# Performance work log

Hardware: AMD Instinct MI355X
Metric: run time of the kernel (lower is better)

Reference implementation:

```python
import jax, jax.numpy as jnp
import numpy as np

N_NODES = 50000
N_EDGES = 625000
H_FEATS = 128


def setup_inputs() -> dict:
    key = jax.random.key(0)
    k_h, k_src, k_dst, k_w1, k_w2 = jax.random.split(key, 5)
    h = jax.random.normal(k_h, (N_NODES, H_FEATS), dtype=jnp.float32)
    src = jax.random.randint(k_src, (N_EDGES,), 0, N_NODES, dtype=jnp.int64)
    dst = jax.random.randint(k_dst, (N_EDGES,), 0, N_NODES, dtype=jnp.int64)
    # Linear weights stored as (in, out) for x @ W + b
    lim1 = 1.0 / np.sqrt(2 * H_FEATS)
    lim2 = 1.0 / np.sqrt(H_FEATS)
    W1 = jax.random.uniform(k_w1, (2 * H_FEATS, H_FEATS), jnp.float32, -lim1, lim1)
    b1 = jnp.zeros((H_FEATS,), jnp.float32)
    W2 = jax.random.uniform(k_w2, (H_FEATS, 1), jnp.float32, -lim2, lim2)
    b2 = jnp.zeros((1,), jnp.float32)
    return {"h": h, "src": src, "dst": dst, "W1": W1, "b1": b1, "W2": W2, "b2": b2}


def reference(h, src, dst, W1, b1, W2, b2):
    # Gather source/destination node features per edge, concat, 2-layer MLP.
    he = jnp.concatenate([h[src], h[dst]], axis=1)          # [E, 2*H]
    hid = jax.nn.relu(he @ W1 + b1)                          # [E, H]
    score = (hid @ W2 + b2)[:, 0]                            # [E]
    return score
```

## Files before the change

### kernel.cpp

```cpp
#include <hip/hip_runtime.h>
#include <hip/hip_bf16.h>

#define N_NODES   50000
#define N_EDGES   625000
#define HF        128
#define MTILE     64
#define NTILES    ((N_EDGES + MTILE - 1) / MTILE)
#define NROWTILES (N_NODES / 16)
#define HB_BYTES  ((size_t)N_NODES * HF * sizeof(short))
#define W1F_BYTES ((size_t)4096 * 16)
#define UVQ_BYTES ((size_t)N_NODES * 256)
#define SCL_BYTES ((size_t)N_NODES * 8)
#define WS_NEED   (W1F_BYTES + UVQ_BYTES + SCL_BYTES)

typedef __attribute__((ext_vector_type(8))) short s16x8;
typedef __attribute__((ext_vector_type(4))) float f32x4;
typedef __attribute__((ext_vector_type(4))) unsigned int u32x4;

__device__ __forceinline__ short f2bf(float x) {
    unsigned u = __builtin_bit_cast(unsigned, x);
    u += 0x7FFFu + ((u >> 16) & 1u);
    return (short)(u >> 16);
}
__device__ __forceinline__ float bf2f(short s) {
    return __builtin_bit_cast(float, ((unsigned)(unsigned short)s) << 16);
}

__global__ void conv_w_kernel(const float* __restrict__ W1, short* __restrict__ w1f) {
    int j = blockIdx.x * 256 + threadIdx.x;
    if (j < 4096) {
        const int lr  = j & 15;
        const int lg  = (j >> 4) & 3;
        const int ntg = (j >> 6) & 15;
        const int kt  = j >> 10;
        const int n2  = ntg * 16 + lr;
        const int kb  = kt * 32 + lg * 8;
        const float* wp = (n2 < 128) ? (W1 + (size_t)kb * 128 + n2)
                                     : (W1 + (size_t)(kb + 128) * 128 + (n2 - 128));
        s16x8 f;
        #pragma unroll
        for (int i = 0; i < 8; ++i) f[i] = f2bf(wp[(size_t)i * 128]);
        ((s16x8*)w1f)[j] = f;
    }
}

__global__ __launch_bounds__(256, 3) void uv_gemm7_kernel(
    const float* __restrict__ h,
    const short* __restrict__ w1f,
    const float* __restrict__ b1,
    unsigned char* __restrict__ UVq,
    float2* __restrict__ scl)
{
    __shared__ short ldsA[16 * 128];
    __shared__ float rm[4][16];
    __shared__ __align__(16) char qt[16][272];

    const int t  = threadIdx.x;
    const int w  = t >> 6;
    const int l  = t & 63;
    const int lg = l >> 4;
    const int lr = l & 15;
    const int srow = t >> 4;
    const int sch  = t & 15;
    const int side = w >> 1;

    s16x8 bfrag[4][4];
    #pragma unroll
    for (int kt = 0; kt < 4; ++kt)
        #pragma unroll
        for (int nt = 0; nt < 4; ++nt)
            bfrag[kt][nt] = ((const s16x8*)w1f)[(kt * 16 + w * 4 + nt) * 64 + l];

    float b1v[4];
    #pragma unroll
    for (int nt = 0; nt < 4; ++nt)
        b1v[nt] = 0.5f * b1[(w * 64 + nt * 16 + lr) & 127];

    int tile = blockIdx.x;
    f32x4 pa, pb;
    {
        int gr = tile * 16 + srow; if (gr > N_NODES - 1) gr = N_NODES - 1;
        const float* hp = h + (size_t)gr * HF + sch * 8;
        pa = *reinterpret_cast<const f32x4*>(hp);
        pb = *reinterpret_cast<const f32x4*>(hp + 4);
    }

    while (tile < NROWTILES) {
        const int R0 = tile * 16;
        {
            s16x8 p;
            p[0]=f2bf(pa[0]); p[1]=f2bf(pa[1]); p[2]=f2bf(pa[2]); p[3]=f2bf(pa[3]);
            p[4]=f2bf(pb[0]); p[5]=f2bf(pb[1]); p[6]=f2bf(pb[2]); p[7]=f2bf(pb[3]);
            *reinterpret_cast<s16x8*>((char*)ldsA + srow * 256 + ((sch * 16) ^ ((srow & 7) << 4))) = p;
        }
        const int next = tile + gridDim.x;
        if (next < NROWTILES) {
            int gr = next * 16 + srow; if (gr > N_NODES - 1) gr = N_NODES - 1;
            const float* hp = h + (size_t)gr * HF + sch * 8;
            pa = *reinterpret_cast<const f32x4*>(hp);
            pb = *reinterpret_cast<const f32x4*>(hp + 4);
        }
        __syncthreads();

        s16x8 afr[4];
        #pragma unroll
        for (int kt = 0; kt < 4; ++kt)
            afr[kt] = *reinterpret_cast<const s16x8*>(
                (char*)ldsA + lr * 256 + ((kt * 64 + lg * 16) ^ ((lr & 7) << 4)));

        f32x4 acc[4];
        #pragma unroll
        for (int nt = 0; nt < 4; ++nt) acc[nt] = (f32x4){0.f, 0.f, 0.f, 0.f};
        #pragma unroll
        for (int kt = 0; kt < 4; ++kt)
            #pragma unroll
            for (int nt = 0; nt < 4; ++nt)
                acc[nt] = __builtin_amdgcn_mfma_f32_16x16x32_bf16(afr[kt], bfrag[kt][nt], acc[nt], 0, 0, 0);

        float val[4][4];
        float am[4];
        #pragma unroll
        for (int rr = 0; rr < 4; ++rr) am[rr] = 0.f;
        #pragma unroll
        for (int nt = 0; nt < 4; ++nt)
            #pragma unroll
            for (int rr = 0; rr < 4; ++rr) {
                float v = acc[nt][rr] + b1v[nt];
                val[nt][rr] = v;
                float a = fabsf(v);
                am[rr] = a > am[rr] ? a : am[rr];
            }
        #pragma unroll
        for (int m = 1; m <= 8; m <<= 1)
            #pragma unroll
            for (int rr = 0; rr < 4; ++rr) {
                float o = __shfl_xor(am[rr], m, 64);
                am[rr] = o > am[rr] ? o : am[rr];
            }
        if (lr == 0) {
            #pragma unroll
            for (int rr = 0; rr < 4; ++rr) rm[w][lg * 4 + rr] = am[rr];
        }
        __syncthreads();

        #pragma unroll
        for (int rr = 0; rr < 4; ++rr) {
            const int row = lg * 4 + rr;
            const float rmax = fmaxf(rm[side * 2][row], rm[side * 2 + 1][row]);
            const float inv = rmax > 0.f ? 127.f / rmax : 0.f;
            #pragma unroll
            for (int nt = 0; nt < 4; ++nt) {
                int q = (int)rintf(val[nt][rr] * inv) + 128;
                q = q < 0 ? 0 : (q > 255 ? 255 : q);
                qt[row][w * 64 + nt * 16 + lr] = (char)q;
            }
        }
        if (t < 16) {
            const float sU = fmaxf(rm[0][t], rm[1][t]) * (1.f / 127.f);
            const float sV = fmaxf(rm[2][t], rm[3][t]) * (1.f / 127.f);
            const int grow = R0 + t;
            if (grow < N_NODES) {
                float2 s2; s2.x = sU; s2.y = sV;
                scl[grow] = s2;
            }
        }
        __syncthreads();

        {
            const int row = t >> 4, ch = t & 15;
            const int grow = R0 + row;
            if (grow < N_NODES) {
                u32x4 vv = *reinterpret_cast<const u32x4*>(&qt[row][ch * 16]);
                *reinterpret_cast<u32x4*>(UVq + (size_t)grow * 256 + ch * 16) = vv;
            }
        }
        __syncthreads();
        tile = next;
    }
}

__device__ __forceinline__ float dot16q(u32x4 u, u32x4 v, float su, float sv,
                                        const float* w2) {
    const float off = -128.f * (su + sv);
    float a = 0.f;
    #pragma unroll
    for (int q = 0; q < 4; ++q) {
        const unsigned uu = u[q], vv = v[q];
        #pragma unroll
        for (int b = 0; b < 4; ++b) {
            const float cu = (float)((uu >> (8 * b)) & 255u);
            const float cv = (float)((vv >> (8 * b)) & 255u);
            float tt = fmaf(su, cu, fmaf(sv, cv, off));
            tt = tt > 0.f ? tt : 0.f;
            a = fmaf(tt, w2[q * 4 + b], a);
        }
    }
    return a;
}

__global__ __launch_bounds__(256) void edge_combine6_kernel(
    const unsigned char* __restrict__ UVq,
    const float2* __restrict__ scl,
    const int*   __restrict__ src,
    const int*   __restrict__ dst,
    const float* __restrict__ W2,
    const float* __restrict__ b2,
    float* __restrict__ out)
{
    const int t  = threadIdx.x;
    const int w  = t >> 6;
    const int l  = t & 63;
    const int eg = l >> 3;
    const int dg = l & 7;

    float w2v[16];
    #pragma unroll
    for (int j = 0; j < 16; ++j) w2v[j] = W2[dg * 16 + j];
    const float b2v = b2[0];

    const int gw = blockIdx.x * 4 + w;
    const int stride = gridDim.x * 4 * 32;

    int base = gw * 32;
    int jj0 = base + (l & 31); if (jj0 > N_EDGES - 1) jj0 = N_EDGES - 1;
    int ids = (l < 32) ? src[jj0] : dst[jj0];

    for (; base < N_EDGES; base += stride) {
        const float2 sc2 = scl[ids];
        const float sval = (l < 32) ? sc2.x : sc2.y;

        const int s0 = __shfl(ids, 0 * 8 + eg, 64), d0 = __shfl(ids, 32 + 0 * 8 + eg, 64);
        const int s1 = __shfl(ids, 1 * 8 + eg, 64), d1 = __shfl(ids, 32 + 1 * 8 + eg, 64);
        const int s2 = __shfl(ids, 2 * 8 + eg, 64), d2 = __shfl(ids, 32 + 2 * 8 + eg, 64);
        const int s3 = __shfl(ids, 3 * 8 + eg, 64), d3 = __shfl(ids, 32 + 3 * 8 + eg, 64);

        u32x4 uq0 = *(const u32x4*)(UVq + (size_t)s0 * 256 + dg * 16);
        u32x4 vq0 = *(const u32x4*)(UVq + (size_t)d0 * 256 + 128 + dg * 16);
        u32x4 uq1 = *(const u32x4*)(UVq + (size_t)s1 * 256 + dg * 16);
        u32x4 vq1 = *(const u32x4*)(UVq + (size_t)d1 * 256 + 128 + dg * 16);
        u32x4 uq2 = *(const u32x4*)(UVq + (size_t)s2 * 256 + dg * 16);
        u32x4 vq2 = *(const u32x4*)(UVq + (size_t)d2 * 256 + 128 + dg * 16);
        u32x4 uq3 = *(const u32x4*)(UVq + (size_t)s3 * 256 + dg * 16);
        u32x4 vq3 = *(const u32x4*)(UVq + (size_t)d3 * 256 + 128 + dg * 16);

        const int nb = base + stride;
        if (nb < N_EDGES) {
            int j2 = nb + (l & 31); if (j2 > N_EDGES - 1) j2 = N_EDGES - 1;
            ids = (l < 32) ? src[j2] : dst[j2];
        }
        __builtin_amdgcn_sched_barrier(0);

        const float su0 = __shfl(sval, 0 * 8 + eg, 64), sv0 = __shfl(sval, 32 + 0 * 8 + eg, 64);
        const float su1 = __shfl(sval, 1 * 8 + eg, 64), sv1 = __shfl(sval, 32 + 1 * 8 + eg, 64);
        const float su2 = __shfl(sval, 2 * 8 + eg, 64), sv2 = __shfl(sval, 32 + 2 * 8 + eg, 64);
        const float su3 = __shfl(sval, 3 * 8 + eg, 64), sv3 = __shfl(sval, 32 + 3 * 8 + eg, 64);

        float a0 = dot16q(uq0, vq0, su0, sv0, w2v);
        float a1 = dot16q(uq1, vq1, su1, sv1, w2v);
        float a2 = dot16q(uq2, vq2, su2, sv2, w2v);
        float a3 = dot16q(uq3, vq3, su3, sv3, w2v);

        #pragma unroll
        for (int m = 1; m <= 4; m <<= 1) {
            a0 += __shfl_xor(a0, m, 64);
            a1 += __shfl_xor(a1, m, 64);
            a2 += __shfl_xor(a2, m, 64);
            a3 += __shfl_xor(a3, m, 64);
        }

        if (dg == 0) {
            if (base + 0 * 8 + eg < N_EDGES) __builtin_nontemporal_store(a0 + b2v, &out[base + 0 * 8 + eg]);
            if (base + 1 * 8 + eg < N_EDGES) __builtin_nontemporal_store(a1 + b2v, &out[base + 1 * 8 + eg]);
            if (base + 2 * 8 + eg < N_EDGES) __builtin_nontemporal_store(a2 + b2v, &out[base + 2 * 8 + eg]);
            if (base + 3 * 8 + eg < N_EDGES) __builtin_nontemporal_store(a3 + b2v, &out[base + 3 * 8 + eg]);
        }
    }
}

__global__ void conv_h_kernel(const float* __restrict__ h, short* __restrict__ hb) {
    int i = blockIdx.x * blockDim.x + threadIdx.x;
    const int n8 = N_NODES * HF / 8;
    if (i < n8) {
        f32x4 a = ((const f32x4*)h)[i * 2];
        f32x4 b = ((const f32x4*)h)[i * 2 + 1];
        s16x8 p;
        p[0]=f2bf(a[0]); p[1]=f2bf(a[1]); p[2]=f2bf(a[2]); p[3]=f2bf(a[3]);
        p[4]=f2bf(b[0]); p[5]=f2bf(b[1]); p[6]=f2bf(b[2]); p[7]=f2bf(b[3]);
        ((s16x8*)hb)[i] = p;
    }
}

__device__ __forceinline__ void gatherA(const short* __restrict__ hb,
                                        int sid, int did, int lg, s16x8 (&A)[8]) {
    const s16x8* bs = (const s16x8*)(hb + (size_t)sid * HF);
    const s16x8* bd = (const s16x8*)(hb + (size_t)did * HF);
    A[0] = bs[lg];      A[1] = bs[4 + lg];  A[2] = bs[8 + lg];  A[3] = bs[12 + lg];
    A[4] = bd[lg];      A[5] = bd[4 + lg];  A[6] = bd[8 + lg];  A[7] = bd[12 + lg];
}

__device__ __forceinline__ void step_tile_v2(
    int tile, int g,
    const short* __restrict__ hb,
    const int* __restrict__ src, const int* __restrict__ dst,
    s16x8 (&Acur)[8], s16x8 (&Anext)[8],
    int sidg, int didg, int& sid2, int& did2,
    const s16x8 (&bfrag)[8][4],
    const float (&b1v)[4], const float (&w2v)[4], float b2v,
    float* __restrict__ out,
    float (&lds_p)[2][2][MTILE], int pp,
    int t, int r, int c, int lg, int lr, int myrow)
{
    gatherA(hb, sidg, didg, lg, Anext);
    {
        int e = (tile + 2 * g) * MTILE + myrow;
        e = e < N_EDGES ? e : N_EDGES - 1;
        sid2 = src[e]; did2 = dst[e];
    }
    f32x4 acc[4];
    #pragma unroll
    for (int nt = 0; nt < 4; ++nt) acc[nt] = (f32x4){0.f, 0.f, 0.f, 0.f};
    #pragma unroll
    for (int kt = 0; kt < 8; ++kt)
        #pragma unroll
        for (int nt = 0; nt < 4; ++nt)
            acc[nt] = __builtin_amdgcn_mfma_f32_16x16x32_bf16(Acur[kt], bfrag[kt][nt], acc[nt], 0, 0, 0);

    float s0[4];
    #pragma unroll
    for (int rr = 0; rr < 4; ++rr) {
        float a = 0.f;
        #pragma unroll
        for (int nt = 0; nt < 4; ++nt) {
            float v = acc[nt][rr] + b1v[nt];
            v = v > 0.f ? v : 0.f;
            a += v * w2v[nt];
        }
        s0[rr] = a;
    }
    #pragma unroll
    for (int mask = 1; mask <= 8; mask <<= 1)
        #pragma unroll
        for (int rr = 0; rr < 4; ++rr)
            s0[rr] += __shfl_xor(s0[rr], mask, 64);

    if (lr == 0) {
        #pragma unroll
        for (int rr = 0; rr < 4; ++rr)
            lds_p[pp][c][r * 16 + lg * 4 + rr] = s0[rr];
    }
    asm volatile("s_waitcnt lgkmcnt(0)" ::: "memory");
    __builtin_amdgcn_s_barrier();
    asm volatile("" ::: "memory");

    if (t < MTILE) {
        int e = tile * MTILE + t;
        if (e < N_EDGES)
            out[e] = lds_p[pp][0][t] + lds_p[pp][1][t] + b2v;
    }
}

__global__ __launch_bounds__(512, 2) void mlp_edge_score_v2(
    const short* __restrict__ hb,
    const int*   __restrict__ src,
    const int*   __restrict__ dst,
    const float* __restrict__ W1,
    const float* __restrict__ b1,
    const float* __restrict__ W2,
    const float* __restrict__ b2,
    float* __restrict__ out)
{
    __shared__ float lds_p[2][2][MTILE];

    const int t  = threadIdx.x;
    const int w  = t >> 6;
    const int l  = t & 63;
    const int r  = w >> 1;
    const int c  = w & 1;
    const int lg = l >> 4;
    const int lr = l & 15;
    const int myrow = r * 16 + lr;

    s16x8 bfrag[8][4];
    #pragma unroll
    for (int kt = 0; kt < 8; ++kt)
        #pragma unroll
        for (int nt = 0; nt < 4; ++nt) {
            const int n  = c * 64 + nt * 16 + lr;
            const int kb = kt * 32 + lg * 8;
            s16x8 f;
            #pragma unroll
            for (int i = 0; i < 8; ++i) f[i] = f2bf(W1[(size_t)(kb + i) * HF + n]);
            bfrag[kt][nt] = f;
        }
    float b1v[4], w2v[4];
    #pragma unroll
    for (int nt = 0; nt < 4; ++nt) {
        const int n = c * 64 + nt * 16 + lr;
        b1v[nt] = b1[n];
        w2v[nt] = W2[n];
    }
    const float b2v = b2[0];

    const int g = gridDim.x;
    const int tile0 = blockIdx.x;

    s16x8 Aa[8], Ab[8];
    {
        int e = tile0 * MTILE + myrow;
        e = e < N_EDGES ? e : N_EDGES - 1;
        gatherA(hb, src[e], dst[e], lg, Aa);
    }
    int sidA, didA, sidB, didB;
    {
        int e = (tile0 + g) * MTILE + myrow;
        e = e < N_EDGES ? e : N_EDGES - 1;
        sidA = src[e]; didA = dst[e];
    }

    int pp = 0;
    for (int tile = tile0; tile < NTILES; tile += 2 * g) {
        step_tile_v2(tile, g, hb, src, dst, Aa, Ab, sidA, didA, sidB, didB,
                     bfrag, b1v, w2v, b2v, out, lds_p, pp, t, r, c, lg, lr, myrow);
        pp ^= 1;
        if (tile + g < NTILES) {
            step_tile_v2(tile + g, g, hb, src, dst, Ab, Aa, sidB, didB, sidA, didA,
                         bfrag, b1v, w2v, b2v, out, lds_p, pp, t, r, c, lg, lr, myrow);
            pp ^= 1;
        }
    }
}

extern "C" void kernel_launch(void* const* d_in, const int* in_sizes, int n_in,
                              void* d_out, int out_size, void* d_ws, size_t ws_size,
                              hipStream_t stream) {
    const float* h   = (const float*)d_in[0];
    const int*   src = (const int*)  d_in[1];
    const int*   dst = (const int*)  d_in[2];
    const float* W1  = (const float*)d_in[3];
    const float* b1  = (const float*)d_in[4];
    const float* W2  = (const float*)d_in[5];
    const float* b2  = (const float*)d_in[6];
    float* out = (float*)d_out;

    if (ws_size >= WS_NEED) {
        char* ws = (char*)d_ws;
        short* w1f = (short*)ws;
        unsigned char* UVq = (unsigned char*)(ws + W1F_BYTES);
        float2* scl = (float2*)(ws + W1F_BYTES + UVQ_BYTES);

        conv_w_kernel<<<16, 256, 0, stream>>>(W1, w1f);
        uv_gemm7_kernel<<<1024, 256, 0, stream>>>(h, w1f, b1, UVq, scl);
        edge_combine6_kernel<<<1024, 256, 0, stream>>>(UVq, scl, src, dst, W2, b2, out);
    } else {
        short* hb = (short*)d_ws;
        const int n8 = N_NODES * HF / 8;
        conv_h_kernel<<<(n8 + 255) / 256, 256, 0, stream>>>(h, hb);
        mlp_edge_score_v2<<<256, 512, 0, stream>>>(hb, src, dst, W1, b1, W2, b2, out);
    }
}
```

Baseline: 48.51 us.

## Process 64 edges per wave with int2 index loads in edge combine

The edge-combine kernel now handles 64 edges per wave per iteration instead of 32. Each lane loads two adjacent src/dst indices as an int2 and two scale pairs. An unrolled loop of 8 edges per 8-lane group then gathers the quantized U/V rows. This drops the software prefetch of the next iteration's indices and the sched_barrier, trading that explicit overlap for more gathers in flight per iteration. Register pressure rises and each iteration's index load is no longer hidden.

Measured after the change: 54.66 us. +12.7%, slower.

```diff
diff --git a/kernel.cpp b/kernel.cpp
--- a/kernel.cpp
+++ b/kernel.cpp
@@ -198,7 +198,7 @@
     return a;
 }
 
-__global__ __launch_bounds__(256) void edge_combine6_kernel(
+__global__ __launch_bounds__(256) void edge_combine8_kernel(
     const unsigned char* __restrict__ UVq,
     const float2* __restrict__ scl,
     const int*   __restrict__ src,
@@ -219,60 +219,37 @@
     const float b2v = b2[0];
 
     const int gw = blockIdx.x * 4 + w;
-    const int stride = gridDim.x * 4 * 32;
-
-    int base = gw * 32;
-    int jj0 = base + (l & 31); if (jj0 > N_EDGES - 1) jj0 = N_EDGES - 1;
-    int ids = (l < 32) ? src[jj0] : dst[jj0];
-
-    for (; base < N_EDGES; base += stride) {
-        const float2 sc2 = scl[ids];
-        const float sval = (l < 32) ? sc2.x : sc2.y;
-
-        const int s0 = __shfl(ids, 0 * 8 + eg, 64), d0 = __shfl(ids, 32 + 0 * 8 + eg, 64);
-        const int s1 = __shfl(ids, 1 * 8 + eg, 64), d1 = __shfl(ids, 32 + 1 * 8 + eg, 64);
-        const int s2 = __shfl(ids, 2 * 8 + eg, 64), d2 = __shfl(ids, 32 + 2 * 8 + eg, 64);
-        const int s3 = __shfl(ids, 3 * 8 + eg, 64), d3 = __shfl(ids, 32 + 3 * 8 + eg, 64);
-
-        u32x4 uq0 = *(const u32x4*)(UVq + (size_t)s0 * 256 + dg * 16);
-        u32x4 vq0 = *(const u32x4*)(UVq + (size_t)d0 * 256 + 128 + dg * 16);
-        u32x4 uq1 = *(const u32x4*)(UVq + (size_t)s1 * 256 + dg * 16);
-        u32x4 vq1 = *(const u32x4*)(UVq + (size_t)d1 * 256 + 128 + dg * 16);
-        u32x4 uq2 = *(const u32x4*)(UVq + (size_t)s2 * 256 + dg * 16);
-        u32x4 vq2 = *(const u32x4*)(UVq + (size_t)d2 * 256 + 128 + dg * 16);
-        u32x4 uq3 = *(const u32x4*)(UVq + (size_t)s3 * 256 + dg * 16);
-        u32x4 vq3 = *(const u32x4*)(UVq + (size_t)d3 * 256 + 128 + dg * 16);
-
-        const int nb = base + stride;
-        if (nb < N_EDGES) {
-            int j2 = nb + (l & 31); if (j2 > N_EDGES - 1) j2 = N_EDGES - 1;
-            ids = (l < 32) ? src[j2] : dst[j2];
-        }
-        __builtin_amdgcn_sched_barrier(0);
-
-        const float su0 = __shfl(sval, 0 * 8 + eg, 64), sv0 = __shfl(sval, 32 + 0 * 8 + eg, 64);
-        const float su1 = __shfl(sval, 1 * 8 + eg, 64), sv1 = __shfl(sval, 32 + 1 * 8 + eg, 64);
-        const float su2 = __shfl(sval, 2 * 8 + eg, 64), sv2 = __shfl(sval, 32 + 2 * 8 + eg, 64);
-        const float su3 = __shfl(sval, 3 * 8 + eg, 64), sv3 = __shfl(sval, 32 + 3 * 8 + eg, 64);
-
-        float a0 = dot16q(uq0, vq0, su0, sv0, w2v);
-        float a1 = dot16q(uq1, vq1, su1, sv1, w2v);
-        float a2 = dot16q(uq2, vq2, su2, sv2, w2v);
-        float a3 = dot16q(uq3, vq3, su3, sv3, w2v);
-
-        #pragma unroll
-        for (int m = 1; m <= 4; m <<= 1) {
-            a0 += __shfl_xor(a0, m, 64);
-            a1 += __shfl_xor(a1, m, 64);
-            a2 += __shfl_xor(a2, m, 64);
-            a3 += __shfl_xor(a3, m, 64);
-        }
-
-        if (dg == 0) {
-            if (base + 0 * 8 + eg < N_EDGES) __builtin_nontemporal_store(a0 + b2v, &out[base + 0 * 8 + eg]);
-            if (base + 1 * 8 + eg < N_EDGES) __builtin_nontemporal_store(a1 + b2v, &out[base + 1 * 8 + eg]);
-            if (base + 2 * 8 + eg < N_EDGES) __builtin_nontemporal_store(a2 + b2v, &out[base + 2 * 8 + eg]);
-            if (base + 3 * 8 + eg < N_EDGES) __builtin_nontemporal_store(a3 + b2v, &out[base + 3 * 8 + eg]);
+    const int stride = gridDim.x * 4 * 64;
+
+    for (int base = gw * 64; base < N_EDGES; base += stride) {
+        int ii = base + 2 * (l & 31);
+        if (ii > N_EDGES - 2) ii = N_EDGES - 2;
+        const int2 id2 = *reinterpret_cast<const int2*>(((l < 32) ? src : dst) + ii);
+
+        const float2 sca = scl[id2.x];
+        const float2 scb = scl[id2.y];
+        const float sv0 = (l < 32) ? sca.x : sca.y;
+        const float sv1 = (l < 32) ? scb.x : scb.y;
+
+        #pragma unroll
+        for (int k = 0; k < 8; ++k) {
+            const int sl = eg * 4 + (k >> 1);
+            const int s  = (k & 1) ? __shfl(id2.y, sl, 64)      : __shfl(id2.x, sl, 64);
+            const int d  = (k & 1) ? __shfl(id2.y, 32 + sl, 64) : __shfl(id2.x, 32 + sl, 64);
+            const float su = (k & 1) ? __shfl(sv1, sl, 64)      : __shfl(sv0, sl, 64);
+            const float sv = (k & 1) ? __shfl(sv1, 32 + sl, 64) : __shfl(sv0, 32 + sl, 64);
+
+            u32x4 uq = *(const u32x4*)(UVq + (size_t)s * 256 + dg * 16);
+            u32x4 vq = *(const u32x4*)(UVq + (size_t)d * 256 + 128 + dg * 16);
+
+            float a = dot16q(uq, vq, su, sv, w2v);
+            a += __shfl_xor(a, 1, 64);
+            a += __shfl_xor(a, 2, 64);
+            a += __shfl_xor(a, 4, 64);
+
+            const int e = base + eg * 8 + k;
+            if (dg == 0 && e < N_EDGES)
+                __builtin_nontemporal_store(a + b2v, &out[e]);
         }
     }
 }
@@ -450,7 +427,7 @@
 
         conv_w_kernel<<<16, 256, 0, stream>>>(W1, w1f);
         uv_gemm7_kernel<<<1024, 256, 0, stream>>>(h, w1f, b1, UVq, scl);
-        edge_combine6_kernel<<<1024, 256, 0, stream>>>(UVq, scl, src, dst, W2, b2, out);
+        edge_combine8_kernel<<<1024, 256, 0, stream>>>(UVq, scl, src, dst, W2, b2, out);
     } else {
         short* hb = (short*)d_ws;
         const int n8 = N_NODES * HF / 8;
```
